# Optimization experiments

Hardware: AMD Instinct MI355X
Metric: run time of the kernel (lower is better)

## Reference

```python
import jax, jax.numpy as jnp
import numpy as np
import math

NUM_HEADS = 16
HEAD_SIZE = 64
HIDDEN = NUM_HEADS * HEAD_SIZE
LN_EPS = 1e-12


def setup_inputs() -> dict:
    key = jax.random.key(0)
    ks = jax.random.split(key, 8)
    B, Lw, Le, H = 8, 512, 64, HIDDEN
    scale = 0.02
    return {
        "word_hidden_states": jax.random.normal(ks[0], (B, Lw, H), jnp.float32),
        "entity_hidden_states": jax.random.normal(ks[1], (B, Le, H), jnp.float32),
        "attention_mask": jnp.zeros((B, 1, 1, Lw + Le), jnp.float32),
        "Wq": jax.random.normal(ks[2], (H, H), jnp.float32) * scale,
        "bq": jnp.zeros((H,), jnp.float32),
        "Wk": jax.random.normal(ks[3], (H, H), jnp.float32) * scale,
        "bk": jnp.zeros((H,), jnp.float32),
        "Wv": jax.random.normal(ks[4], (H, H), jnp.float32) * scale,
        "bv": jnp.zeros((H,), jnp.float32),
        "Wo": jax.random.normal(ks[5], (H, H), jnp.float32) * scale,
        "bo": jnp.zeros((H,), jnp.float32),
        "ln_w": jnp.ones((H,), jnp.float32),
        "ln_b": jnp.zeros((H,), jnp.float32),
    }


def _layernorm(x, w, b):
    u = jnp.mean(x, axis=-1, keepdims=True)
    s = jnp.mean(jnp.square(x - u), axis=-1, keepdims=True)
    return w * ((x - u) / jnp.sqrt(s + LN_EPS)) + b


def reference(word_hidden_states, entity_hidden_states, attention_mask,
              Wq, bq, Wk, bk, Wv, bv, Wo, bo, ln_w, ln_b):
    B, Lw, H = word_hidden_states.shape
    x = jnp.concatenate([word_hidden_states, entity_hidden_states], axis=1)  # [B,S,H]
    S = x.shape[1]

    def heads(t):  # [B,S,H] -> [B,nh,S,hd]
        return t.reshape(B, S, NUM_HEADS, HEAD_SIZE).transpose(0, 2, 1, 3)

    q = heads(x @ Wq + bq)
    k = heads(x @ Wk + bk)
    v = heads(x @ Wv + bv)

    scores = jnp.einsum("bhqd,bhkd->bhqk", q, k) / math.sqrt(HEAD_SIZE)
    scores = scores + attention_mask  # additive mask, broadcast [B,1,1,S]
    probs = jax.nn.softmax(scores, axis=-1)
    ctx = jnp.einsum("bhqk,bhkd->bhqd", probs, v)
    ctx = ctx.transpose(0, 2, 1, 3).reshape(B, S, H)

    # SelfOutput (shared weights) applied per-stream; equivalent on concat since
    # residual is the concatenated input and LayerNorm is per-token.
    out = _layernorm(ctx @ Wo + bo + x, ln_w, ln_b)
    return out[:, :Lw, :], out[:, Lw:, :]
```

## Files before the change

kernel.cpp:

```cpp
#include <hip/hip_runtime.h>

#define NHEADS 16
#define HDIM   64
#define HID    1024
#define BATCH  8
#define LW     512
#define LE     64
#define SEQ    576
#define MTOT   (BATCH * SEQ)

typedef unsigned short u16;
typedef __bf16 bf16x8 __attribute__((ext_vector_type(8)));
typedef float  f32x4  __attribute__((ext_vector_type(4)));

__device__ __forceinline__ u16 f2bf(float f) {
  union { float f; unsigned int i; } x;
  x.f = f;
  unsigned int u = x.i;
  unsigned int r = (u + 0x7FFFu + ((u >> 16) & 1u)) >> 16;
  return (u16)r;
}
__device__ __forceinline__ unsigned int pk2(float a, float b) {
  return (unsigned int)f2bf(a) | ((unsigned int)f2bf(b) << 16);
}

__device__ __forceinline__ void gload16(const u16* g, u16* l) {
  __builtin_amdgcn_global_load_lds(
      (const __attribute__((address_space(1))) void*)g,
      (__attribute__((address_space(3))) void*)l, 16, 0, 0);
}

__global__ __launch_bounds__(256) void prep_k(
    const float* __restrict__ w0, const float* __restrict__ w1,
    const float* __restrict__ w2, const float* __restrict__ w3,
    u16* __restrict__ wt,
    const float* __restrict__ word, const float* __restrict__ ent,
    u16* __restrict__ xb)
{
  const int bid = blockIdx.x, tid = threadIdx.x;
  if (bid < 4096) {
    __shared__ u16 tile[32][33];
    const int z = bid >> 10, rem = bid & 1023;
    const int bx = rem & 31, by = rem >> 5;
    const float* src = (z == 0) ? w0 : (z == 1) ? w1 : (z == 2) ? w2 : w3;
    u16* dst = wt + (size_t)z * HID * HID;
    const int tx = tid & 31, ty = tid >> 5;
    const int nx = bx * 32, ky = by * 32;
#pragma unroll
    for (int j = 0; j < 4; ++j)
      tile[ty * 4 + j][tx] = f2bf(src[(size_t)(ky + ty * 4 + j) * HID + nx + tx]);
    __syncthreads();
#pragma unroll
    for (int j = 0; j < 4; ++j)
      dst[(size_t)(nx + ty * 4 + j) * HID + ky + tx] = tile[tx][ty * 4 + j];
  } else {
    const int row = bid - 4096;
    const int bb = row / SEQ, ss = row - bb * SEQ;
    const float* src = (ss < LW) ? word + (size_t)(bb * LW + ss) * HID
                                 : ent  + (size_t)(bb * LE + (ss - LW)) * HID;
    float4 v = *(const float4*)(src + tid * 4);
    ushort4 o;
    o.x = f2bf(v.x); o.y = f2bf(v.y); o.z = f2bf(v.z); o.w = f2bf(v.w);
    *(ushort4*)(xb + (size_t)row * HID + tid * 4) = o;
  }
}

__global__ __launch_bounds__(256) void qkv_gemm_k(
    const u16* __restrict__ xb, const u16* __restrict__ wt,
    const float* __restrict__ bq, const float* __restrict__ bk, const float* __restrict__ bv,
    u16* __restrict__ q_ws, u16* __restrict__ k_ws, u16* __restrict__ v_ws)
{
  __shared__ u16 sh[4 * 64 * 68];
  const int which = blockIdx.z;
  const u16* W = wt + (size_t)which * HID * HID;
  const float* bias = (which == 0) ? bq : (which == 1) ? bk : bv;
  const int m0 = blockIdx.x * 128, n0 = blockIdx.y * 128;
  const int tid = threadIdx.x, lane = tid & 63, wv = tid >> 6;
  const int lr = lane & 15, quad = lane >> 4;
  const int wm = (wv >> 1) * 64, wn = (wv & 1) * 64;
  const int srow = wv * 16 + (lane >> 2);
  const int gseg = ((lane & 3) ^ ((lane >> 4) & 3)) * 8;
  const int lseg = (lane & 3) * 8;
  const u16* gA = xb + (size_t)(m0 + srow) * HID + gseg;
  const u16* gB = W + (size_t)(n0 + srow) * HID + gseg;
  const int fc = (quad ^ (lr >> 2)) * 8;

  const f32x4 fz = {0.f, 0.f, 0.f, 0.f};
  f32x4 acc[4][4];
#pragma unroll
  for (int a = 0; a < 4; ++a)
#pragma unroll
    for (int b = 0; b < 4; ++b) acc[a][b] = fz;

  {
    u16* As = sh; u16* Bs = sh + 4096;
    gload16(gA, As + srow * 32 + lseg);
    gload16(gA + (size_t)64 * HID, As + 2048 + srow * 32 + lseg);
    gload16(gB, Bs + srow * 32 + lseg);
    gload16(gB + (size_t)64 * HID, Bs + 2048 + srow * 32 + lseg);
  }
  for (int ki = 0; ki < 32; ++ki) {
    const int cur = ki & 1;
    __syncthreads();
    if (ki + 1 < 32) {
      const int k0 = (ki + 1) * 32;
      u16* As = sh + (cur ^ 1) * 8192; u16* Bs = As + 4096;
      gload16(gA + k0, As + srow * 32 + lseg);
      gload16(gA + (size_t)64 * HID + k0, As + 2048 + srow * 32 + lseg);
      gload16(gB + k0, Bs + srow * 32 + lseg);
      gload16(gB + (size_t)64 * HID + k0, Bs + 2048 + srow * 32 + lseg);
    }
    u16* As = sh + cur * 8192; u16* Bs = As + 4096;
    bf16x8 af[4], bfr[4];
#pragma unroll
    for (int i = 0; i < 4; ++i) {
      af[i]  = *(const bf16x8*)(&As[(wm + i * 16 + lr) * 32 + fc]);
      bfr[i] = *(const bf16x8*)(&Bs[(wn + i * 16 + lr) * 32 + fc]);
    }
    if (which < 2) {
#pragma unroll
      for (int a = 0; a < 4; ++a)
#pragma unroll
        for (int b = 0; b < 4; ++b)
          acc[a][b] = __builtin_amdgcn_mfma_f32_16x16x32_bf16(bfr[a], af[b], acc[a][b], 0, 0, 0);
    } else {
#pragma unroll
      for (int a = 0; a < 4; ++a)
#pragma unroll
        for (int b = 0; b < 4; ++b)
          acc[a][b] = __builtin_amdgcn_mfma_f32_16x16x32_bf16(af[a], bfr[b], acc[a][b], 0, 0, 0);
    }
  }
  __syncthreads();

  u16* tb = sh + wv * (64 * 68);
  const int head = (n0 + wn) >> 6;
  const int mbase = m0 + wm;
  const int bb = mbase / SEQ;
  const int ssb = mbase - bb * SEQ;

  if (which < 2) {
    float4 bias4[4];
#pragma unroll
    for (int ni = 0; ni < 4; ++ni)
      bias4[ni] = *(const float4*)(bias + n0 + wn + ni * 16 + quad * 4);
#pragma unroll
    for (int mi = 0; mi < 4; ++mi)
#pragma unroll
      for (int ni = 0; ni < 4; ++ni) {
        uint2 w2v;
        w2v.x = pk2(acc[ni][mi][0] + bias4[ni].x, acc[ni][mi][1] + bias4[ni].y);
        w2v.y = pk2(acc[ni][mi][2] + bias4[ni].z, acc[ni][mi][3] + bias4[ni].w);
        *(uint2*)(&tb[(mi * 16 + lr) * 68 + ni * 16 + quad * 4]) = w2v;
      }
    u16* drow = (which == 0 ? q_ws : k_ws)
              + ((size_t)(bb * NHEADS + head) * SEQ + ssb) * HDIM;
#pragma unroll
    for (int i = 0; i < 8; ++i) {
      int rrow = i * 8 + (lane >> 3);
      int seg = lane & 7;
      bf16x8 v8 = *(const bf16x8*)(&tb[rrow * 68 + seg * 8]);
      *(bf16x8*)(drow + (size_t)rrow * HDIM + seg * 8) = v8;
    }
  } else {
    float bcol[4];
#pragma unroll
    for (int ni = 0; ni < 4; ++ni) bcol[ni] = bias[n0 + wn + ni * 16 + lr];
#pragma unroll
    for (int mi = 0; mi < 4; ++mi)
#pragma unroll
      for (int ni = 0; ni < 4; ++ni) {
        uint2 w2v;
        w2v.x = pk2(acc[mi][ni][0] + bcol[ni], acc[mi][ni][1] + bcol[ni]);
        w2v.y = pk2(acc[mi][ni][2] + bcol[ni], acc[mi][ni][3] + bcol[ni]);
        *(uint2*)(&tb[(ni * 16 + lr) * 68 + (mi >> 1) * 32 + quad * 8 + (mi & 1) * 4]) = w2v;
      }
    u16* dcol = v_ws + ((size_t)(bb * NHEADS + head) * HDIM) * SEQ + ssb;
#pragma unroll
    for (int i = 0; i < 8; ++i) {
      int d = i * 8 + (lane >> 3);
      int seg = lane & 7;
      bf16x8 v8 = *(const bf16x8*)(&tb[d * 68 + seg * 8]);
      *(bf16x8*)(dcol + (size_t)d * SEQ + seg * 8) = v8;
    }
  }
}

__global__ __launch_bounds__(256) void attn_k(
    const u16* __restrict__ q_ws, const u16* __restrict__ k_ws,
    const u16* __restrict__ v_ws, const float* __restrict__ mask,
    u16* __restrict__ ctxh)
{
  __shared__ u16 Ks[2][4096];
  __shared__ u16 Vs[2][4096];
  __shared__ float ms[576];
  const int bhx = blockIdx.x, qt = blockIdx.y;
  const int b = bhx >> 4, h = bhx & 15;
  const int tid = threadIdx.x, lane = tid & 63, wv = tid >> 6;
  const int lr = lane & 15, quad = lane >> 4;
  const int q0 = qt * 64 + wv * 16;
  const u16* kbh = k_ws + (size_t)bhx * SEQ * HDIM;
  const u16* vbh = v_ws + (size_t)bhx * HDIM * SEQ;
  const u16* qp  = q_ws + ((size_t)bhx * SEQ + q0) * HDIM;
  const float* mrow = mask + b * SEQ;

  if (tid < 144) *(float4*)(&ms[tid * 4]) = *(const float4*)(mrow + tid * 4);

  const int subrow = lane >> 3;
  const int gsw = (lane & 7) ^ subrow;

  bf16x8 qf[2];
  qf[0] = *(const bf16x8*)(qp + lr * HDIM + quad * 8);
  qf[1] = *(const bf16x8*)(qp + lr * HDIM + 32 + quad * 8);

  const f32x4 fz = {0.f, 0.f, 0.f, 0.f};
  f32x4 oa[4] = {fz, fz, fz, fz};
  f32x4 rsv = fz;
  const int fA = lr & 7;

#pragma unroll
  for (int j = 0; j < 2; ++j) {
    int row = (wv * 2 + j) * 8 + subrow;
    gload16(kbh + (size_t)row * HDIM + gsw * 8, &Ks[0][((wv * 2 + j) * 64 + lane) * 8]);
    gload16(vbh + (size_t)row * SEQ + gsw * 8,  &Vs[0][((wv * 2 + j) * 64 + lane) * 8]);
  }

  for (int ci = 0; ci < 9; ++ci) {
    const int cur = ci & 1;
    const int c = ci * 64;
    __syncthreads();
    if (ci + 1 < 9) {
      int cn = c + 64;
#pragma unroll
      for (int j = 0; j < 2; ++j) {
        int row = (wv * 2 + j) * 8 + subrow;
        gload16(kbh + ((size_t)(cn + row)) * HDIM + gsw * 8,
                &Ks[cur ^ 1][((wv * 2 + j) * 64 + lane) * 8]);
        gload16(vbh + (size_t)row * SEQ + cn + gsw * 8,
                &Vs[cur ^ 1][((wv * 2 + j) * 64 + lane) * 8]);
      }
    }
    f32x4 s[4] = {fz, fz, fz, fz};
#pragma unroll
    for (int ks = 0; ks < 2; ++ks)
#pragma unroll
      for (int t = 0; t < 4; ++t) {
        bf16x8 kf = *(const bf16x8*)(&Ks[cur][(t * 16 + lr) * 64 + (((ks * 4 + quad) ^ fA) * 8)]);
        s[t] = __builtin_amdgcn_mfma_f32_16x16x32_bf16(kf, qf[ks], s[t], 0, 0, 0);
      }
    unsigned int pk0[4], pk1[4];
#pragma unroll
    for (int t = 0; t < 4; ++t) {
      float4 mv = *(const float4*)(&ms[c + t * 16 + quad * 4]);
      s[t][0] = __expf(s[t][0] * 0.125f + mv.x);
      s[t][1] = __expf(s[t][1] * 0.125f + mv.y);
      s[t][2] = __expf(s[t][2] * 0.125f + mv.z);
      s[t][3] = __expf(s[t][3] * 0.125f + mv.w);
      rsv += s[t];
      pk0[t] = pk2(s[t][0], s[t][1]);
      pk1[t] = pk2(s[t][2], s[t][3]);
    }
#pragma unroll
    for (int ks = 0; ks < 2; ++ks) {
      union { unsigned int u[4]; bf16x8 v; } ap;
      ap.u[0] = pk0[ks * 2];     ap.u[1] = pk1[ks * 2];
      ap.u[2] = pk0[ks * 2 + 1]; ap.u[3] = pk1[ks * 2 + 1];
#pragma unroll
      for (int n = 0; n < 4; ++n) {
        bf16x8 vf = *(const bf16x8*)(&Vs[cur][(n * 16 + lr) * 64 + (((ks * 4 + quad) ^ fA) * 8)]);
        oa[n] = __builtin_amdgcn_mfma_f32_16x16x32_bf16(ap.v, vf, oa[n], 0, 0, 0);
      }
    }
  }

  float rl = rsv[0] + rsv[1] + rsv[2] + rsv[3];
  rl += __shfl_xor(rl, 16);
  rl += __shfl_xor(rl, 32);
  float inv = 1.0f / rl;
  float invr[4];
#pragma unroll
  for (int r = 0; r < 4; ++r) invr[r] = __shfl(inv, quad * 4 + r);

  u16* pw = (wv < 2) ? &Ks[1][wv * 2048] : &Vs[1][(wv - 2) * 2048];
#pragma unroll
  for (int n = 0; n < 4; ++n)
#pragma unroll
    for (int r = 0; r < 4; ++r)
      pw[(quad * 4 + r) * 68 + n * 16 + lr] = f2bf(oa[n][r] * invr[r]);
  const int token0 = b * SEQ + q0;
  u16* cb = ctxh + ((size_t)h * MTOT + token0) * HDIM;
#pragma unroll
  for (int i = 0; i < 2; ++i) {
    int row = lane & 15;
    int seg = (lane >> 4) + i * 4;
    bf16x8 v8 = *(const bf16x8*)(&pw[row * 68 + seg * 8]);
    *(bf16x8*)(cb + (size_t)row * HDIM + seg * 8) = v8;
  }
}

__global__ __launch_bounds__(256) void out_gemm_k(
    const u16* __restrict__ ctxh, const u16* __restrict__ wto,
    const float* __restrict__ bo,
    const float* __restrict__ word, const float* __restrict__ ent,
    float* __restrict__ y)
{
  __shared__ u16 sh[16384];
  const int m0 = blockIdx.x * 128, n0 = blockIdx.y * 128;
  const int tid = threadIdx.x, lane = tid & 63, wv = tid >> 6;
  const int lr = lane & 15, quad = lane >> 4;
  const int wm = (wv >> 1) * 64, wn = (wv & 1) * 64;
  const int srow = wv * 16 + (lane >> 2);
  const int gseg = ((lane & 3) ^ ((lane >> 4) & 3)) * 8;
  const int lseg = (lane & 3) * 8;
  const u16* gB = wto + (size_t)(n0 + srow) * HID + gseg;
  const int fc = (quad ^ (lr >> 2)) * 8;

  const f32x4 fz = {0.f, 0.f, 0.f, 0.f};
  f32x4 acc[4][4];
#pragma unroll
  for (int mi = 0; mi < 4; ++mi)
#pragma unroll
    for (int ni = 0; ni < 4; ++ni) acc[mi][ni] = fz;

  {
    u16* As = sh; u16* Bs = sh + 4096;
    gload16(ctxh + ((size_t)0 * MTOT + (m0 + srow)) * HDIM + 0 + gseg, As + srow * 32 + lseg);
    gload16(ctxh + ((size_t)0 * MTOT + (m0 + 64 + srow)) * HDIM + 0 + gseg, As + 2048 + srow * 32 + lseg);
    gload16(gB, Bs + srow * 32 + lseg);
    gload16(gB + (size_t)64 * HID, Bs + 2048 + srow * 32 + lseg);
  }
  for (int ki = 0; ki < 32; ++ki) {
    const int cur = ki & 1;
    __syncthreads();
    if (ki + 1 < 32) {
      const int k0 = (ki + 1) * 32;
      const int hblk = k0 >> 6, koff = k0 & 63;
      u16* As = sh + (cur ^ 1) * 8192; u16* Bs = As + 4096;
      gload16(ctxh + ((size_t)hblk * MTOT + (m0 + srow)) * HDIM + koff + gseg, As + srow * 32 + lseg);
      gload16(ctxh + ((size_t)hblk * MTOT + (m0 + 64 + srow)) * HDIM + koff + gseg, As + 2048 + srow * 32 + lseg);
      gload16(gB + k0, Bs + srow * 32 + lseg);
      gload16(gB + (size_t)64 * HID + k0, Bs + 2048 + srow * 32 + lseg);
    }
    u16* As = sh + cur * 8192; u16* Bs = As + 4096;
    bf16x8 af[4], bfr[4];
#pragma unroll
    for (int i = 0; i < 4; ++i) {
      af[i]  = *(const bf16x8*)(&As[(wm + i * 16 + lr) * 32 + fc]);
      bfr[i] = *(const bf16x8*)(&Bs[(wn + i * 16 + lr) * 32 + fc]);
    }
#pragma unroll
    for (int mi = 0; mi < 4; ++mi)
#pragma unroll
      for (int ni = 0; ni < 4; ++ni)
        acc[mi][ni] = __builtin_amdgcn_mfma_f32_16x16x32_bf16(af[mi], bfr[ni], acc[mi][ni], 0, 0, 0);
  }

#pragma unroll
  for (int mi = 0; mi < 4; ++mi) {
    int rowb = m0 + wm + mi * 16 + quad * 4;
#pragma unroll
    for (int r = 0; r < 4; ++r) {
      int row = rowb + r;
      int bb = row / SEQ, ss = row - bb * SEQ;
      const float* res = (ss < LW) ? (word + (size_t)(bb * LW + ss) * HID)
                                   : (ent  + (size_t)(bb * LE + (ss - LW)) * HID);
#pragma unroll
      for (int ni = 0; ni < 4; ++ni) {
        int col = n0 + wn + ni * 16 + lr;
        y[(size_t)row * HID + col] = acc[mi][ni][r] + bo[col] + res[col];
      }
    }
  }
}

__global__ __launch_bounds__(256) void ln_k(
    const float* __restrict__ y, const float* __restrict__ lnw,
    const float* __restrict__ lnb, float* __restrict__ out)
{
  const int row = blockIdx.x;
  const int tid = threadIdx.x;
  __shared__ float ssum[4], sqq[4];

  const float* yr = y + (size_t)row * HID;
  float4 v = *(const float4*)(yr + tid * 4);
  float s = v.x + v.y + v.z + v.w;
  float q = v.x * v.x + v.y * v.y + v.z * v.z + v.w * v.w;
#pragma unroll
  for (int o = 32; o > 0; o >>= 1) { s += __shfl_xor(s, o); q += __shfl_xor(q, o); }
  if ((tid & 63) == 0) { ssum[tid >> 6] = s; sqq[tid >> 6] = q; }
  __syncthreads();
  s = ssum[0] + ssum[1] + ssum[2] + ssum[3];
  q = sqq[0] + sqq[1] + sqq[2] + sqq[3];
  float mean = s * (1.0f / HID);
  float var  = q * (1.0f / HID) - mean * mean;
  float rstd = rsqrtf(var + 1e-12f);

  int bb = row / SEQ, ss2 = row - bb * SEQ;
  float* dst = (ss2 < LW)
             ? out + (size_t)(bb * LW + ss2) * HID
             : out + (size_t)BATCH * LW * HID + (size_t)(bb * LE + (ss2 - LW)) * HID;

  float4 w4 = *(const float4*)(lnw + tid * 4);
  float4 b4 = *(const float4*)(lnb + tid * 4);
  float4 o4;
  o4.x = w4.x * (v.x - mean) * rstd + b4.x;
  o4.y = w4.y * (v.y - mean) * rstd + b4.y;
  o4.z = w4.z * (v.z - mean) * rstd + b4.z;
  o4.w = w4.w * (v.w - mean) * rstd + b4.w;
  *(float4*)(dst + tid * 4) = o4;
}

extern "C" void kernel_launch(void* const* d_in, const int* in_sizes, int n_in,
                              void* d_out, int out_size, void* d_ws, size_t ws_size,
                              hipStream_t stream) {
  const float* word = (const float*)d_in[0];
  const float* ent  = (const float*)d_in[1];
  const float* mask = (const float*)d_in[2];
  const float* Wq   = (const float*)d_in[3];
  const float* bq   = (const float*)d_in[4];
  const float* Wk   = (const float*)d_in[5];
  const float* bk   = (const float*)d_in[6];
  const float* Wv   = (const float*)d_in[7];
  const float* bv   = (const float*)d_in[8];
  const float* Wo   = (const float*)d_in[9];
  const float* bo   = (const float*)d_in[10];
  const float* lnw  = (const float*)d_in[11];
  const float* lnb  = (const float*)d_in[12];

  char* base = (char*)d_ws;
  u16*   wt   = (u16*)base;
  u16*   q_ws = (u16*)(base + (size_t)8 * 1024 * 1024);
  u16*   k_ws = q_ws + (size_t)MTOT * HID;
  u16*   v_ws = k_ws + (size_t)MTOT * HID;
  u16*   ctxh = v_ws + (size_t)MTOT * HID;
  char*  xy   = (char*)(ctxh + (size_t)MTOT * HID);
  u16*   xb   = (u16*)xy;
  float* y    = (float*)xy;

  hipLaunchKernelGGL(prep_k, dim3(4096 + MTOT), dim3(256), 0, stream,
                     Wq, Wk, Wv, Wo, wt, word, ent, xb);
  hipLaunchKernelGGL(qkv_gemm_k, dim3(MTOT / 128, HID / 128, 3), dim3(256), 0, stream,
                     xb, wt, bq, bk, bv, q_ws, k_ws, v_ws);
  hipLaunchKernelGGL(attn_k, dim3(BATCH * NHEADS, SEQ / 64), dim3(256), 0, stream,
                     q_ws, k_ws, v_ws, mask, ctxh);
  hipLaunchKernelGGL(out_gemm_k, dim3(MTOT / 128, HID / 128), dim3(256), 0, stream,
                     ctxh, wt + (size_t)3 * HID * HID, bo, word, ent, y);
  hipLaunchKernelGGL(ln_k, dim3(MTOT), dim3(256), 0, stream,
                     y, lnw, lnb, (float*)d_out);
}
```

Before: 203.6 us.

## Load GEMM MFMA fragments directly from global memory, dropping LDS staging

Both the QKV projection and output projection GEMMs stop staging A/B tiles through double-buffered shared memory with async loads and barriers. Each wave now reads its bf16x8 MFMA fragments straight from global memory, relying on L1/L2 caches for reuse between waves. This removes the per-iteration __syncthreads and LDS traffic. In exchange each block issues about twice the global/cache reads and loses explicit prefetch overlap, so it may become more latency-bound.

```diff
diff --git a/kernel.cpp b/kernel.cpp
--- a/kernel.cpp
+++ b/kernel.cpp
@@ -78,12 +78,9 @@
   const int tid = threadIdx.x, lane = tid & 63, wv = tid >> 6;
   const int lr = lane & 15, quad = lane >> 4;
   const int wm = (wv >> 1) * 64, wn = (wv & 1) * 64;
-  const int srow = wv * 16 + (lane >> 2);
-  const int gseg = ((lane & 3) ^ ((lane >> 4) & 3)) * 8;
-  const int lseg = (lane & 3) * 8;
-  const u16* gA = xb + (size_t)(m0 + srow) * HID + gseg;
-  const u16* gB = W + (size_t)(n0 + srow) * HID + gseg;
-  const int fc = (quad ^ (lr >> 2)) * 8;
+
+  const u16* gA = xb + (size_t)(m0 + wm + lr) * HID + quad * 8;
+  const u16* gB = W  + (size_t)(n0 + wn + lr) * HID + quad * 8;
 
   const f32x4 fz = {0.f, 0.f, 0.f, 0.f};
   f32x4 acc[4][4];
@@ -92,30 +89,13 @@
 #pragma unroll
     for (int b = 0; b < 4; ++b) acc[a][b] = fz;
 
-  {
-    u16* As = sh; u16* Bs = sh + 4096;
-    gload16(gA, As + srow * 32 + lseg);
-    gload16(gA + (size_t)64 * HID, As + 2048 + srow * 32 + lseg);
-    gload16(gB, Bs + srow * 32 + lseg);
-    gload16(gB + (size_t)64 * HID, Bs + 2048 + srow * 32 + lseg);
-  }
-  for (int ki = 0; ki < 32; ++ki) {
-    const int cur = ki & 1;
-    __syncthreads();
-    if (ki + 1 < 32) {
-      const int k0 = (ki + 1) * 32;
-      u16* As = sh + (cur ^ 1) * 8192; u16* Bs = As + 4096;
-      gload16(gA + k0, As + srow * 32 + lseg);
-      gload16(gA + (size_t)64 * HID + k0, As + 2048 + srow * 32 + lseg);
-      gload16(gB + k0, Bs + srow * 32 + lseg);
-      gload16(gB + (size_t)64 * HID + k0, Bs + 2048 + srow * 32 + lseg);
-    }
-    u16* As = sh + cur * 8192; u16* Bs = As + 4096;
+#pragma unroll 2
+  for (int k0 = 0; k0 < HID; k0 += 32) {
     bf16x8 af[4], bfr[4];
 #pragma unroll
     for (int i = 0; i < 4; ++i) {
-      af[i]  = *(const bf16x8*)(&As[(wm + i * 16 + lr) * 32 + fc]);
-      bfr[i] = *(const bf16x8*)(&Bs[(wn + i * 16 + lr) * 32 + fc]);
+      af[i]  = *(const bf16x8*)(gA + (size_t)(i * 16) * HID + k0);
+      bfr[i] = *(const bf16x8*)(gB + (size_t)(i * 16) * HID + k0);
     }
     if (which < 2) {
 #pragma unroll
@@ -131,7 +111,6 @@
           acc[a][b] = __builtin_amdgcn_mfma_f32_16x16x32_bf16(af[a], bfr[b], acc[a][b], 0, 0, 0);
     }
   }
-  __syncthreads();
 
   u16* tb = sh + wv * (64 * 68);
   const int head = (n0 + wn) >> 6;
@@ -304,16 +283,12 @@
     const float* __restrict__ word, const float* __restrict__ ent,
     float* __restrict__ y)
 {
-  __shared__ u16 sh[16384];
   const int m0 = blockIdx.x * 128, n0 = blockIdx.y * 128;
   const int tid = threadIdx.x, lane = tid & 63, wv = tid >> 6;
   const int lr = lane & 15, quad = lane >> 4;
   const int wm = (wv >> 1) * 64, wn = (wv & 1) * 64;
-  const int srow = wv * 16 + (lane >> 2);
-  const int gseg = ((lane & 3) ^ ((lane >> 4) & 3)) * 8;
-  const int lseg = (lane & 3) * 8;
-  const u16* gB = wto + (size_t)(n0 + srow) * HID + gseg;
-  const int fc = (quad ^ (lr >> 2)) * 8;
+
+  const u16* gB = wto + (size_t)(n0 + wn + lr) * HID + quad * 8;
 
   const f32x4 fz = {0.f, 0.f, 0.f, 0.f};
   f32x4 acc[4][4];
@@ -322,31 +297,15 @@
 #pragma unroll
     for (int ni = 0; ni < 4; ++ni) acc[mi][ni] = fz;
 
-  {
-    u16* As = sh; u16* Bs = sh + 4096;
-    gload16(ctxh + ((size_t)0 * MTOT + (m0 + srow)) * HDIM + 0 + gseg, As + srow * 32 + lseg);
-    gload16(ctxh + ((size_t)0 * MTOT + (m0 + 64 + srow)) * HDIM + 0 + gseg, As + 2048 + srow * 32 + lseg);
-    gload16(gB, Bs + srow * 32 + lseg);
-    gload16(gB + (size_t)64 * HID, Bs + 2048 + srow * 32 + lseg);
-  }
-  for (int ki = 0; ki < 32; ++ki) {
-    const int cur = ki & 1;
-    __syncthreads();
-    if (ki + 1 < 32) {
-      const int k0 = (ki + 1) * 32;
-      const int hblk = k0 >> 6, koff = k0 & 63;
-      u16* As = sh + (cur ^ 1) * 8192; u16* Bs = As + 4096;
-      gload16(ctxh + ((size_t)hblk * MTOT + (m0 + srow)) * HDIM + koff + gseg, As + srow * 32 + lseg);
-      gload16(ctxh + ((size_t)hblk * MTOT + (m0 + 64 + srow)) * HDIM + koff + gseg, As + 2048 + srow * 32 + lseg);
-      gload16(gB + k0, Bs + srow * 32 + lseg);
-      gload16(gB + (size_t)64 * HID + k0, Bs + 2048 + srow * 32 + lseg);
-    }
-    u16* As = sh + cur * 8192; u16* Bs = As + 4096;
+#pragma unroll 2
+  for (int k0 = 0; k0 < HID; k0 += 32) {
+    const int hblk = k0 >> 6, koff = k0 & 63;
     bf16x8 af[4], bfr[4];
 #pragma unroll
     for (int i = 0; i < 4; ++i) {
-      af[i]  = *(const bf16x8*)(&As[(wm + i * 16 + lr) * 32 + fc]);
-      bfr[i] = *(const bf16x8*)(&Bs[(wn + i * 16 + lr) * 32 + fc]);
+      af[i]  = *(const bf16x8*)(ctxh + ((size_t)hblk * MTOT + (m0 + wm + i * 16 + lr)) * HDIM
+                                + koff + quad * 8);
+      bfr[i] = *(const bf16x8*)(gB + (size_t)(i * 16) * HID + k0);
     }
 #pragma unroll
     for (int mi = 0; mi < 4; ++mi)
```

After: 313.2 us. +53.8%, slower.
